# Kernel optimization log

Hardware: AMD Instinct MI355X
Metric: run time of the kernel (lower is better)

## Reference

```python
import jax, jax.numpy as jnp
import numpy as np

B, NSTEP, NSAMPLE = 16, 32, 10
EMBED, STATE, VOCAB, TOTAL = 128, 512, 32000, 8192
STD_SCALE = 0.113
EPS = 1e-5


def setup_inputs() -> dict:
    key = jax.random.key(0)
    ks = jax.random.split(key, 9)
    g = lambda k, shape: jax.random.normal(k, shape, jnp.float32) * 0.05
    return {
        "zi": jax.random.randint(ks[0], (B,), 0, TOTAL),
        "y": jax.random.randint(ks[1], (B, NSTEP), 0, VOCAB),
        "rd": jax.random.uniform(ks[2], (NSTEP, B, NSAMPLE), jnp.float32),
        "latent": g(ks[3], (TOTAL, EMBED)),
        "state_pref_W": g(ks[4], (STATE, 2 * EMBED)),
        "state_pref_b": g(ks[5], (STATE,)),
        "state_move": g(ks[6], (STATE, EMBED)),
        "vocab_W": g(ks[7], (VOCAB, EMBED)),
        "vocab_b": g(ks[8], (VOCAB,)),
    }


def reference(zi, y, rd, latent, state_pref_W, state_pref_b, state_move, vocab_W, vocab_b):
    # z: [B, NSAMPLE, D] -- latent row per batch element, repeated over samples
    z0 = jnp.repeat(latent[zi][:, None, :], NSAMPLE, axis=1)

    def step(carry, rd_t):
        z, zold, lp = carry
        # per-step normalization (torch std is unbiased, ddof=1)
        z = z / (EPS + jnp.std(z, axis=-1, ddof=1, keepdims=True)) * STD_SCALE
        pref = jnp.concatenate([zold, z], axis=-1) @ state_pref_W.T + state_pref_b  # [B,S,STATE]
        xp = jax.nn.softmax(pref, axis=-1)
        xpc = jnp.cumsum(xp, axis=-1)
        # first index where rd < cumulative prob (argmax of bool = first True)
        which = jnp.argmax(rd_t[:, :, None] < xpc, axis=-1)  # [B,S]
        xps = jnp.take_along_axis(xp, which[:, :, None], axis=-1)[..., 0]
        lp = lp + jnp.log(xps)
        mvs = state_move[which]  # [B,S,D]
        return (z + mvs, z, mvs), mvs

    init = (z0, jnp.zeros_like(z0), jnp.zeros((B, NSAMPLE), jnp.float32))
    # note: carry slot 2 of init is lp=0; fix tuple to match step outputs
    init = (z0, jnp.zeros_like(z0), jnp.zeros((B, NSAMPLE), jnp.float32))

    def step_fixed(carry, rd_t):
        z, zold, lp = carry
        z = z / (EPS + jnp.std(z, axis=-1, ddof=1, keepdims=True)) * STD_SCALE
        pref = jnp.concatenate([zold, z], axis=-1) @ state_pref_W.T + state_pref_b
        xp = jax.nn.softmax(pref, axis=-1)
        xpc = jnp.cumsum(xp, axis=-1)
        which = jnp.argmax(rd_t[:, :, None] < xpc, axis=-1)
        xps = jnp.take_along_axis(xp, which[:, :, None], axis=-1)[..., 0]
        lp = lp + jnp.log(xps)
        mvs = state_move[which]
        return (z + mvs, z, lp), mvs

    (_, _, lp), emits = jax.lax.scan(step_fixed, init, rd)  # emits: [T,B,S,D]
    emits = jnp.transpose(emits, (1, 0, 2, 3))  # [B,T,S,D]
    ys = jax.nn.log_softmax(emits @ vocab_W.T + vocab_b, axis=-1)  # [B,T,S,V]
    idx = jnp.broadcast_to(y[:, :, None, None], (B, NSTEP, NSAMPLE, 1))
    yp = jnp.take_along_axis(ys, idx, axis=-1)[..., 0]  # [B,T,S]
    return yp.mean(axis=2)  # [B,T]
```

## Files before the change

### kernel.cpp

```cpp
#include <hip/hip_runtime.h>
#include <hip/hip_bf16.h>

#define B_ 16
#define T_ 32
#define NS_ 10
#define D_ 128
#define ST_ 512
#define V_ 32000
#define NCHAIN 160

using short8  = __attribute__((ext_vector_type(8))) short;
using f32x4   = __attribute__((ext_vector_type(4))) float;
using half8   = __attribute__((ext_vector_type(8))) _Float16;
using half2v  = __attribute__((ext_vector_type(2))) _Float16;

__device__ __forceinline__ unsigned short f2bf(float f){
  unsigned u = __float_as_uint(f);
  u += 0x7FFFu + ((u >> 16) & 1u);
  return (unsigned short)(u >> 16);
}
__device__ __forceinline__ unsigned packbf(float a, float b){
  return ((unsigned)f2bf(b) << 16) | (unsigned)f2bf(a);
}
__device__ __forceinline__ unsigned short f2h(float f){
  return __builtin_bit_cast(unsigned short, (_Float16)f);
}
__device__ __forceinline__ float h2f(unsigned u, int hi){
  half2v h = __builtin_bit_cast(half2v, u);
  return (float)h[hi];
}
__device__ __forceinline__ float readlane_f(float v, int lane){
  return __int_as_float(__builtin_amdgcn_readlane(__float_as_int(v), lane));
}

#define DPPADD(x, ctrl, rm) { \
  int _t = __builtin_amdgcn_update_dpp(0, __float_as_int(x), ctrl, rm, 0xf, true); \
  x += __int_as_float(_t); }

__global__ __launch_bounds__(256) void prep_kernel(
    const int* __restrict__ zi, const float* __restrict__ latent,
    const float* __restrict__ prefW, const float* __restrict__ move,
    unsigned short* __restrict__ Hh, unsigned short* __restrict__ Lh,
    unsigned short* __restrict__ Gh,
    float* __restrict__ HU0, float* __restrict__ LU0, float* __restrict__ D0,
    float2* __restrict__ S0, float2* __restrict__ SM,
    unsigned* __restrict__ mbf, float* __restrict__ partial)
{
  if (blockIdx.x < 48){
    const int sg = blockIdx.x / 6, vc = blockIdx.x % 6;
    const int wv = threadIdx.x >> 6, lane = threadIdx.x & 63;
    const int c16 = lane & 15, q = lane >> 4;

    half8 afr[4][4];
    #pragma unroll
    for (int rt = 0; rt < 4; ++rt){
      const float* mp = move + (sg*64 + rt*16 + c16)*D_ + q*8;
      #pragma unroll
      for (int kk = 0; kk < 4; ++kk){
        float4 f0 = *(const float4*)(mp + kk*32);
        float4 f1 = *(const float4*)(mp + kk*32 + 4);
        half8 a;
        a[0]=(_Float16)f0.x; a[1]=(_Float16)f0.y; a[2]=(_Float16)f0.z; a[3]=(_Float16)f0.w;
        a[4]=(_Float16)f1.x; a[5]=(_Float16)f1.y; a[6]=(_Float16)f1.z; a[7]=(_Float16)f1.w;
        afr[rt][kk] = a;
      }
    }
    for (int it = 0; it < 4; ++it){
      const int ct = vc*256 + it*64 + wv*16 + c16;
      const float* bp; unsigned short* base; int ccol;
      if (ct < 512)      { bp = prefW + ct*256 + 128; base = Hh; ccol = ct; }
      else if (ct < 1024){ bp = prefW + (ct-512)*256; base = Lh; ccol = ct-512; }
      else               { bp = move + (ct-1024)*128; base = Gh; ccol = ct-1024; }
      half8 bfr[4];
      #pragma unroll
      for (int kk = 0; kk < 4; ++kk){
        float4 f0 = *(const float4*)(bp + q*8 + kk*32);
        float4 f1 = *(const float4*)(bp + q*8 + kk*32 + 4);
        half8 bb;
        bb[0]=(_Float16)f0.x; bb[1]=(_Float16)f0.y; bb[2]=(_Float16)f0.z; bb[3]=(_Float16)f0.w;
        bb[4]=(_Float16)f1.x; bb[5]=(_Float16)f1.y; bb[6]=(_Float16)f1.z; bb[7]=(_Float16)f1.w;
        bfr[kk] = bb;
      }
      #pragma unroll
      for (int rt = 0; rt < 4; ++rt){
        f32x4 acc = {0.f,0.f,0.f,0.f};
        #pragma unroll
        for (int kk = 0; kk < 4; ++kk)
          acc = __builtin_amdgcn_mfma_f32_16x16x32_f16(afr[rt][kk], bfr[kk], acc, 0, 0, 0);
        #pragma unroll
        for (int r = 0; r < 4; ++r){
          const int w = sg*64 + rt*16 + q*4 + r;
          base[w*ST_ + ccol] = f2h(acc[r]);
        }
      }
    }
  } else {
    const int b = blockIdx.x - 48, t = threadIdx.x;
    __shared__ float zl[128];
    if (t < 128) zl[t] = latent[zi[b]*D_ + t];
    __syncthreads();

    #pragma unroll
    for (int ii = 0; ii < 2; ++ii){
      const int sidx = t + ii*256;
      const float* wr = prefW + sidx*256;
      const float* mv = move + sidx*128;
      float hu = 0.f, lu = 0.f, d0 = 0.f;
      #pragma unroll 8
      for (int j = 0; j < 128; j += 4){
        float4 w0 = *(const float4*)(wr + j);
        float4 w1 = *(const float4*)(wr + 128 + j);
        float4 m  = *(const float4*)(mv + j);
        float4 z  = *(const float4*)(&zl[j]);
        lu += w0.x*z.x + w0.y*z.y + w0.z*z.z + w0.w*z.w;
        hu += w1.x*z.x + w1.y*z.y + w1.z*z.z + w1.w*z.w;
        d0 += m.x*z.x + m.y*z.y + m.z*z.z + m.w*z.w;
      }
      HU0[b*ST_ + sidx] = hu; LU0[b*ST_ + sidx] = lu; D0[b*ST_ + sidx] = d0;
    }
    if (t < 64){
      float a = zl[t], bb = zl[t + 64];
      float s1 = a + bb, s2 = a*a + bb*bb;
      #pragma unroll
      for (int m = 1; m < 64; m <<= 1){ s1 += __shfl_xor(s1, m, 64); s2 += __shfl_xor(s2, m, 64); }
      if (t == 0) S0[b] = make_float2(s1, s2);
    }
    {
      const int w = b*32 + (t >> 3);
      const float* mw = move + w*128 + (t & 7)*16;
      float4 m0 = *(const float4*)(mw),   m1 = *(const float4*)(mw+4);
      float4 m2 = *(const float4*)(mw+8), m3 = *(const float4*)(mw+12);
      float s1 = m0.x+m0.y+m0.z+m0.w + m1.x+m1.y+m1.z+m1.w
               + m2.x+m2.y+m2.z+m2.w + m3.x+m3.y+m3.z+m3.w;
      float s2 = m0.x*m0.x+m0.y*m0.y+m0.z*m0.z+m0.w*m0.w
               + m1.x*m1.x+m1.y*m1.y+m1.z*m1.z+m1.w*m1.w
               + m2.x*m2.x+m2.y*m2.y+m2.z*m2.z+m2.w*m2.w
               + m3.x*m3.x+m3.y*m3.y+m3.z*m3.z+m3.w*m3.w;
      #pragma unroll
      for (int m = 1; m < 8; m <<= 1){ s1 += __shfl_xor(s1, m, 64); s2 += __shfl_xor(s2, m, 64); }
      if ((t & 7) == 0) SM[w] = make_float2(s1, s2);
      unsigned* dst = mbf + w*64 + (t & 7)*8;
      dst[0] = packbf(m0.x,m0.y); dst[1] = packbf(m0.z,m0.w);
      dst[2] = packbf(m1.x,m1.y); dst[3] = packbf(m1.z,m1.w);
      dst[4] = packbf(m2.x,m2.y); dst[5] = packbf(m2.z,m2.w);
      dst[6] = packbf(m3.x,m3.y); dst[7] = packbf(m3.z,m3.w);
    }
    if (t < 32) partial[b*32 + t] = 0.f;
  }
}

__global__ __launch_bounds__(256) void work_kernel(
    const unsigned short* __restrict__ Hh, const unsigned short* __restrict__ Lh,
    const unsigned short* __restrict__ Gh, const float2* __restrict__ SM,
    const float* __restrict__ HU0, const float* __restrict__ LU0,
    const float* __restrict__ D0, const float2* __restrict__ S0,
    const float* __restrict__ prefB, const float* __restrict__ rd,
    int* __restrict__ whichOut,
    const unsigned* __restrict__ mbf, const float* __restrict__ vw,
    const float* __restrict__ vb, float* __restrict__ partial)
{
  __shared__ float les[2048];

  if (blockIdx.x < NCHAIN){
    const int t = threadIdx.x;
    if (t >= 64) return;
    const int c = blockIdx.x, b = c / NS_;
    const int l = t, t0 = l*8;

    float HU[8], LU[8], D[8], prev1[8], bias[8];
    #pragma unroll
    for (int k = 0; k < 8; k += 4){
      float4 h = *(const float4*)(HU0 + b*ST_ + t0 + k);
      float4 u = *(const float4*)(LU0 + b*ST_ + t0 + k);
      float4 d = *(const float4*)(D0  + b*ST_ + t0 + k);
      float4 bb= *(const float4*)(prefB + t0 + k);
      HU[k]=h.x; HU[k+1]=h.y; HU[k+2]=h.z; HU[k+3]=h.w;
      LU[k]=u.x; LU[k+1]=u.y; LU[k+2]=u.z; LU[k+3]=u.w;
      D[k]=d.x;  D[k+1]=d.y;  D[k+2]=d.z;  D[k+3]=d.w;
      bias[k]=bb.x; bias[k+1]=bb.y; bias[k+2]=bb.z; bias[k+3]=bb.w;
    }
    #pragma unroll
    for (int k = 0; k < 8; ++k) prev1[k] = 0.f;
    float2 s0 = S0[b];
    float S1 = s0.x, S2 = s0.y;
    float rdreg = (l < T_) ? rd[l*(B_*NS_) + c] : 0.f;

    for (int st = 0; st < T_; ++st){
      const float mean = S1 * (1.f/128.f);
      const float var  = (S2 - 128.f*mean*mean) * (1.f/127.f);
      const float sc   = 0.113f / (1e-5f + sqrtf(var));

      float cum[8]; float run = 0.f;
      #pragma unroll
      for (int k = 0; k < 8; ++k){
        float pref = fmaf(sc, HU[k], prev1[k] + bias[k]);
        run += __expf(pref);
        cum[k] = run;
      }
      float incl = run;
      DPPADD(incl, 0x111, 0xf)
      DPPADD(incl, 0x112, 0xf)
      DPPADD(incl, 0x114, 0xf)
      DPPADD(incl, 0x118, 0xf)
      DPPADD(incl, 0x142, 0xa)
      DPPADD(incl, 0x143, 0xc)
      const float total  = readlane_f(incl, 63);
      const float target = readlane_f(rdreg, st) * total;

      const bool cond = target < incl;
      const unsigned long long bal = __ballot(cond);
      const float excl = incl - run;
      int kw = 7; float dcand = D[7];
      #pragma unroll
      for (int k = 6; k >= 0; --k){
        bool ck = target < excl + cum[k];
        kw = ck ? k : kw;
        dcand = ck ? D[k] : dcand;
      }
      int which; float dW;
      if (bal){
        const int wlane = __ffsll(bal) - 1;
        which = __builtin_amdgcn_readlane(t0 + kw, wlane);
        dW    = readlane_f(dcand, wlane);
      } else {
        which = 0;
        dW    = readlane_f(D[0], 0);
      }
      if (l == 0) whichOut[c*T_ + st] = which;

      const int rb = which*ST_ + t0;
      const uint4 hq = *(const uint4*)(Hh + rb);
      const uint4 lq = *(const uint4*)(Lh + rb);
      const uint4 gq = *(const uint4*)(Gh + rb);
      const float2 sm = SM[which];
      const unsigned ha[4] = {hq.x, hq.y, hq.z, hq.w};
      const unsigned la[4] = {lq.x, lq.y, lq.z, lq.w};
      const unsigned ga[4] = {gq.x, gq.y, gq.z, gq.w};
      #pragma unroll
      for (int k = 0; k < 8; ++k){
        const float Hk = h2f(ha[k>>1], k&1);
        const float Lk = h2f(la[k>>1], k&1);
        const float Gk = h2f(ga[k>>1], k&1);
        const float p1 = sc * LU[k];
        HU[k] = fmaf(sc, HU[k], Hk);
        LU[k] = p1 + Lk;
        D[k]  = fmaf(sc, D[k], Gk);
        prev1[k] = p1;
      }
      S1 = fmaf(sc, S1, sm.x);
      S2 = fmaf(sc*sc, S2, fmaf(2.f*sc, dW, sm.y));
    }
  } else {
    const int t = threadIdx.x, lane = t & 63, wv = t >> 6;
    const int lblk = blockIdx.x - NCHAIN;

    const int vbase = lblk*128 + wv*32;
    short8 afr[2][4];
    float vbr[2][4];
    #pragma unroll
    for (int vt = 0; vt < 2; ++vt){
      const int vr = vbase + vt*16 + (lane & 15);
      const float* wp = vw + vr*D_ + (lane >> 4)*8;
      #pragma unroll
      for (int kk = 0; kk < 4; ++kk){
        float4 f0 = *(const float4*)(wp + kk*32);
        float4 f1 = *(const float4*)(wp + kk*32 + 4);
        short8 a;
        a[0]=(short)f2bf(f0.x); a[1]=(short)f2bf(f0.y);
        a[2]=(short)f2bf(f0.z); a[3]=(short)f2bf(f0.w);
        a[4]=(short)f2bf(f1.x); a[5]=(short)f2bf(f1.y);
        a[6]=(short)f2bf(f1.z); a[7]=(short)f2bf(f1.w);
        afr[vt][kk] = a;
      }
      #pragma unroll
      for (int r = 0; r < 4; ++r)
        vbr[vt][r] = vb[vbase + vt*16 + (lane >> 4)*4 + r];
    }

    const char* mb = (const char*)mbf;
    float esl[32];
    #pragma unroll
    for (int s = 0; s < 32; ++s) esl[s] = 0.f;

    #pragma unroll 4
    for (int s = 0; s < 32; ++s){
      short8 bfr[4];
      #pragma unroll
      for (int kk = 0; kk < 4; ++kk){
        const int row = s*16 + (lane & 15);
        bfr[kk] = *(const short8*)(mb + row*256 + (lane >> 4)*16 + kk*64);
      }
      #pragma unroll
      for (int vt = 0; vt < 2; ++vt){
        f32x4 acc = {0.f,0.f,0.f,0.f};
        #pragma unroll
        for (int kk = 0; kk < 4; ++kk)
          acc = __builtin_amdgcn_mfma_f32_16x16x32_bf16(afr[vt][kk], bfr[kk], acc, 0, 0, 0);
        #pragma unroll
        for (int r = 0; r < 4; ++r)
          esl[s] += __expf(acc[r] + vbr[vt][r]);
      }
    }
    #pragma unroll
    for (int s = 0; s < 32; ++s){
      esl[s] += __shfl_xor(esl[s], 16, 64);
      esl[s] += __shfl_xor(esl[s], 32, 64);
    }
    if (lane < 16){
      #pragma unroll
      for (int s = 0; s < 32; ++s) les[wv*512 + s*16 + lane] = esl[s];
    }
    __syncthreads();
    #pragma unroll
    for (int i = 0; i < 2; ++i){
      const int st = t + i*256;
      atomicAdd(&partial[st], les[st] + les[512+st] + les[1024+st] + les[1536+st]);
    }
  }
}

__global__ __launch_bounds__(256) void dots_kernel(
    const int* __restrict__ whichIn, const int* __restrict__ y,
    const float* __restrict__ move, const float* __restrict__ vw,
    const float* __restrict__ vb, const float* __restrict__ partial,
    float* __restrict__ out)
{
  const int p = blockIdx.x*4 + (threadIdx.x >> 6);
  const int lane = threadIdx.x & 63;
  const int b = p >> 5, st = p & 31;

  int w10 = 0; float ls = 0.f;
  if (lane < NS_){
    w10 = whichIn[(b*NS_ + lane)*T_ + st];
    ls  = __logf(partial[w10]);
  }
  #pragma unroll
  for (int m = 1; m < 16; m <<= 1) ls += __shfl_xor(ls, m, 64);

  float mv0 = 0.f, mv1 = 0.f;
  #pragma unroll
  for (int s = 0; s < NS_; ++s){
    const int ws = __builtin_amdgcn_readlane(w10, s);
    mv0 += move[ws*D_ + lane];
    mv1 += move[ws*D_ + 64 + lane];
  }
  const int yr = y[b*T_ + st];
  float pacc = mv0*vw[yr*D_ + lane] + mv1*vw[yr*D_ + 64 + lane];
  #pragma unroll
  for (int m = 1; m < 64; m <<= 1) pacc += __shfl_xor(pacc, m, 64);
  if (lane == 0) out[b*T_ + st] = (pacc - ls) * (1.f/NS_) + vb[yr];
}

extern "C" void kernel_launch(void* const* d_in, const int* in_sizes, int n_in,
                              void* d_out, int out_size, void* d_ws, size_t ws_size,
                              hipStream_t stream)
{
  const int*   zi     = (const int*)d_in[0];
  const int*   y      = (const int*)d_in[1];
  const float* rd     = (const float*)d_in[2];
  const float* latent = (const float*)d_in[3];
  const float* prefW  = (const float*)d_in[4];
  const float* prefB  = (const float*)d_in[5];
  const float* move   = (const float*)d_in[6];
  const float* vw     = (const float*)d_in[7];
  const float* vb     = (const float*)d_in[8];
  float* out = (float*)d_out;

  char* ws = (char*)d_ws;
  unsigned short* Hh = (unsigned short*)(ws);
  unsigned short* Lh = (unsigned short*)(ws + 524288);
  unsigned short* Gh = (unsigned short*)(ws + 1048576);
  float2* SM    = (float2*)(ws + 1572864);
  float*  HU0   = (float*)(ws + 1576960);
  float*  LU0   = (float*)(ws + 1609728);
  float*  D0    = (float*)(ws + 1642496);
  float2* S0    = (float2*)(ws + 1675264);
  float*  partial = (float*)(ws + 1675392);
  int*    which = (int*)(ws + 1677440);
  unsigned* mbf = (unsigned*)(ws + 1697920);

  hipLaunchKernelGGL(prep_kernel, dim3(64), dim3(256), 0, stream,
                     zi, latent, prefW, move, Hh, Lh, Gh,
                     HU0, LU0, D0, S0, SM, mbf, partial);
  hipLaunchKernelGGL(work_kernel, dim3(NCHAIN + 250), dim3(256), 0, stream,
                     Hh, Lh, Gh, SM, HU0, LU0, D0, S0, prefB, rd, which,
                     mbf, vw, vb, partial);
  hipLaunchKernelGGL(dots_kernel, dim3(128), dim3(256), 0, stream,
                     which, y, move, vw, vb, partial, out);
}
```

Baseline: 65.13 us.

## Fuse prep, work and dots kernels into one cooperative kernel with grid syncs

Merges the three launches into one cooperative kernel of 256 blocks, with grid-wide syncs between the prep, chain/logsumexp and output phases. If the cooperative launch fails it falls back to three launches of the same kernel. The prep matmul is spread over 192 blocks instead of 48, and the vocab logsumexp work is looped over 96 blocks instead of 250. This is meant to remove launch gaps, at the cost of grid-sync overhead and fewer blocks for the vocab phase, which now runs concurrently with the serial chains.

```diff
diff --git a/kernel.cpp b/kernel.cpp
--- a/kernel.cpp
+++ b/kernel.cpp
@@ -1,5 +1,8 @@
 #include <hip/hip_runtime.h>
 #include <hip/hip_bf16.h>
+#include <hip/hip_cooperative_groups.h>
+
+namespace cg = cooperative_groups;
 
 #define B_ 16
 #define T_ 32
@@ -8,6 +11,7 @@
 #define ST_ 512
 #define V_ 32000
 #define NCHAIN 160
+#define NBLK 256
 
 using short8  = __attribute__((ext_vector_type(8))) short;
 using f32x4   = __attribute__((ext_vector_type(4))) float;
@@ -37,36 +41,42 @@
   int _t = __builtin_amdgcn_update_dpp(0, __float_as_int(x), ctrl, rm, 0xf, true); \
   x += __int_as_float(_t); }
 
-__global__ __launch_bounds__(256) void prep_kernel(
-    const int* __restrict__ zi, const float* __restrict__ latent,
-    const float* __restrict__ prefW, const float* __restrict__ move,
+__global__ __launch_bounds__(256) void fused_kernel(
+    const int* __restrict__ zi, const int* __restrict__ y,
+    const float* __restrict__ rd, const float* __restrict__ latent,
+    const float* __restrict__ prefW, const float* __restrict__ prefB,
+    const float* __restrict__ move, const float* __restrict__ vw,
+    const float* __restrict__ vb,
     unsigned short* __restrict__ Hh, unsigned short* __restrict__ Lh,
-    unsigned short* __restrict__ Gh,
+    unsigned short* __restrict__ Gh, float2* __restrict__ SM,
     float* __restrict__ HU0, float* __restrict__ LU0, float* __restrict__ D0,
-    float2* __restrict__ S0, float2* __restrict__ SM,
-    unsigned* __restrict__ mbf, float* __restrict__ partial)
+    float2* __restrict__ S0, float* __restrict__ partial,
+    int* __restrict__ whichOut, unsigned* __restrict__ mbf,
+    float* __restrict__ out, int coop, int phase)
 {
-  if (blockIdx.x < 48){
-    const int sg = blockIdx.x / 6, vc = blockIdx.x % 6;
-    const int wv = threadIdx.x >> 6, lane = threadIdx.x & 63;
-    const int c16 = lane & 15, q = lane >> 4;
-
-    half8 afr[4][4];
-    #pragma unroll
-    for (int rt = 0; rt < 4; ++rt){
-      const float* mp = move + (sg*64 + rt*16 + c16)*D_ + q*8;
-      #pragma unroll
-      for (int kk = 0; kk < 4; ++kk){
-        float4 f0 = *(const float4*)(mp + kk*32);
-        float4 f1 = *(const float4*)(mp + kk*32 + 4);
-        half8 a;
-        a[0]=(_Float16)f0.x; a[1]=(_Float16)f0.y; a[2]=(_Float16)f0.z; a[3]=(_Float16)f0.w;
-        a[4]=(_Float16)f1.x; a[5]=(_Float16)f1.y; a[6]=(_Float16)f1.z; a[7]=(_Float16)f1.w;
-        afr[rt][kk] = a;
-      }
-    }
-    for (int it = 0; it < 4; ++it){
-      const int ct = vc*256 + it*64 + wv*16 + c16;
+  __shared__ float les[2048];
+  const int bid = blockIdx.x, t = threadIdx.x;
+  const int lane = t & 63, wv = t >> 6;
+  const int c16 = lane & 15, q = lane >> 4;
+
+  if (phase & 1){
+    if (bid < 192){
+      const int sg = bid / 24, tile = bid % 24;
+      half8 afr[4][4];
+      #pragma unroll
+      for (int rt = 0; rt < 4; ++rt){
+        const float* mp = move + (sg*64 + rt*16 + c16)*D_ + q*8;
+        #pragma unroll
+        for (int kk = 0; kk < 4; ++kk){
+          float4 f0 = *(const float4*)(mp + kk*32);
+          float4 f1 = *(const float4*)(mp + kk*32 + 4);
+          half8 a;
+          a[0]=(_Float16)f0.x; a[1]=(_Float16)f0.y; a[2]=(_Float16)f0.z; a[3]=(_Float16)f0.w;
+          a[4]=(_Float16)f1.x; a[5]=(_Float16)f1.y; a[6]=(_Float16)f1.z; a[7]=(_Float16)f1.w;
+          afr[rt][kk] = a;
+        }
+      }
+      const int ct = tile*64 + wv*16 + c16;
       const float* bp; unsigned short* base; int ccol;
       if (ct < 512)      { bp = prefW + ct*256 + 128; base = Hh; ccol = ct; }
       else if (ct < 1024){ bp = prefW + (ct-512)*256; base = Lh; ccol = ct-512; }
@@ -93,262 +103,251 @@
           base[w*ST_ + ccol] = f2h(acc[r]);
         }
       }
-    }
-  } else {
-    const int b = blockIdx.x - 48, t = threadIdx.x;
-    __shared__ float zl[128];
-    if (t < 128) zl[t] = latent[zi[b]*D_ + t];
-    __syncthreads();
-
-    #pragma unroll
-    for (int ii = 0; ii < 2; ++ii){
-      const int sidx = t + ii*256;
-      const float* wr = prefW + sidx*256;
-      const float* mv = move + sidx*128;
-      float hu = 0.f, lu = 0.f, d0 = 0.f;
-      #pragma unroll 8
-      for (int j = 0; j < 128; j += 4){
-        float4 w0 = *(const float4*)(wr + j);
-        float4 w1 = *(const float4*)(wr + 128 + j);
-        float4 m  = *(const float4*)(mv + j);
-        float4 z  = *(const float4*)(&zl[j]);
-        lu += w0.x*z.x + w0.y*z.y + w0.z*z.z + w0.w*z.w;
-        hu += w1.x*z.x + w1.y*z.y + w1.z*z.z + w1.w*z.w;
-        d0 += m.x*z.x + m.y*z.y + m.z*z.z + m.w*z.w;
-      }
-      HU0[b*ST_ + sidx] = hu; LU0[b*ST_ + sidx] = lu; D0[b*ST_ + sidx] = d0;
-    }
-    if (t < 64){
-      float a = zl[t], bb = zl[t + 64];
-      float s1 = a + bb, s2 = a*a + bb*bb;
-      #pragma unroll
-      for (int m = 1; m < 64; m <<= 1){ s1 += __shfl_xor(s1, m, 64); s2 += __shfl_xor(s2, m, 64); }
-      if (t == 0) S0[b] = make_float2(s1, s2);
-    }
-    {
-      const int w = b*32 + (t >> 3);
-      const float* mw = move + w*128 + (t & 7)*16;
-      float4 m0 = *(const float4*)(mw),   m1 = *(const float4*)(mw+4);
-      float4 m2 = *(const float4*)(mw+8), m3 = *(const float4*)(mw+12);
-      float s1 = m0.x+m0.y+m0.z+m0.w + m1.x+m1.y+m1.z+m1.w
-               + m2.x+m2.y+m2.z+m2.w + m3.x+m3.y+m3.z+m3.w;
-      float s2 = m0.x*m0.x+m0.y*m0.y+m0.z*m0.z+m0.w*m0.w
-               + m1.x*m1.x+m1.y*m1.y+m1.z*m1.z+m1.w*m1.w
-               + m2.x*m2.x+m2.y*m2.y+m2.z*m2.z+m2.w*m2.w
-               + m3.x*m3.x+m3.y*m3.y+m3.z*m3.z+m3.w*m3.w;
-      #pragma unroll
-      for (int m = 1; m < 8; m <<= 1){ s1 += __shfl_xor(s1, m, 64); s2 += __shfl_xor(s2, m, 64); }
-      if ((t & 7) == 0) SM[w] = make_float2(s1, s2);
-      unsigned* dst = mbf + w*64 + (t & 7)*8;
-      dst[0] = packbf(m0.x,m0.y); dst[1] = packbf(m0.z,m0.w);
-      dst[2] = packbf(m1.x,m1.y); dst[3] = packbf(m1.z,m1.w);
-      dst[4] = packbf(m2.x,m2.y); dst[5] = packbf(m2.z,m2.w);
-      dst[6] = packbf(m3.x,m3.y); dst[7] = packbf(m3.z,m3.w);
-    }
-    if (t < 32) partial[b*32 + t] = 0.f;
-  }
-}
-
-__global__ __launch_bounds__(256) void work_kernel(
-    const unsigned short* __restrict__ Hh, const unsigned short* __restrict__ Lh,
-    const unsigned short* __restrict__ Gh, const float2* __restrict__ SM,
-    const float* __restrict__ HU0, const float* __restrict__ LU0,
-    const float* __restrict__ D0, const float2* __restrict__ S0,
-    const float* __restrict__ prefB, const float* __restrict__ rd,
-    int* __restrict__ whichOut,
-    const unsigned* __restrict__ mbf, const float* __restrict__ vw,
-    const float* __restrict__ vb, float* __restrict__ partial)
-{
-  __shared__ float les[2048];
-
-  if (blockIdx.x < NCHAIN){
-    const int t = threadIdx.x;
-    if (t >= 64) return;
-    const int c = blockIdx.x, b = c / NS_;
-    const int l = t, t0 = l*8;
-
-    float HU[8], LU[8], D[8], prev1[8], bias[8];
-    #pragma unroll
-    for (int k = 0; k < 8; k += 4){
-      float4 h = *(const float4*)(HU0 + b*ST_ + t0 + k);
-      float4 u = *(const float4*)(LU0 + b*ST_ + t0 + k);
-      float4 d = *(const float4*)(D0  + b*ST_ + t0 + k);
-      float4 bb= *(const float4*)(prefB + t0 + k);
-      HU[k]=h.x; HU[k+1]=h.y; HU[k+2]=h.z; HU[k+3]=h.w;
-      LU[k]=u.x; LU[k+1]=u.y; LU[k+2]=u.z; LU[k+3]=u.w;
-      D[k]=d.x;  D[k+1]=d.y;  D[k+2]=d.z;  D[k+3]=d.w;
-      bias[k]=bb.x; bias[k+1]=bb.y; bias[k+2]=bb.z; bias[k+3]=bb.w;
-    }
-    #pragma unroll
-    for (int k = 0; k < 8; ++k) prev1[k] = 0.f;
-    float2 s0 = S0[b];
-    float S1 = s0.x, S2 = s0.y;
-    float rdreg = (l < T_) ? rd[l*(B_*NS_) + c] : 0.f;
-
-    for (int st = 0; st < T_; ++st){
-      const float mean = S1 * (1.f/128.f);
-      const float var  = (S2 - 128.f*mean*mean) * (1.f/127.f);
-      const float sc   = 0.113f / (1e-5f + sqrtf(var));
-
-      float cum[8]; float run = 0.f;
-      #pragma unroll
-      for (int k = 0; k < 8; ++k){
-        float pref = fmaf(sc, HU[k], prev1[k] + bias[k]);
-        run += __expf(pref);
-        cum[k] = run;
-      }
-      float incl = run;
-      DPPADD(incl, 0x111, 0xf)
-      DPPADD(incl, 0x112, 0xf)
-      DPPADD(incl, 0x114, 0xf)
-      DPPADD(incl, 0x118, 0xf)
-      DPPADD(incl, 0x142, 0xa)
-      DPPADD(incl, 0x143, 0xc)
-      const float total  = readlane_f(incl, 63);
-      const float target = readlane_f(rdreg, st) * total;
-
-      const bool cond = target < incl;
-      const unsigned long long bal = __ballot(cond);
-      const float excl = incl - run;
-      int kw = 7; float dcand = D[7];
-      #pragma unroll
-      for (int k = 6; k >= 0; --k){
-        bool ck = target < excl + cum[k];
-        kw = ck ? k : kw;
-        dcand = ck ? D[k] : dcand;
-      }
-      int which; float dW;
-      if (bal){
-        const int wlane = __ffsll(bal) - 1;
-        which = __builtin_amdgcn_readlane(t0 + kw, wlane);
-        dW    = readlane_f(dcand, wlane);
-      } else {
-        which = 0;
-        dW    = readlane_f(D[0], 0);
-      }
-      if (l == 0) whichOut[c*T_ + st] = which;
-
-      const int rb = which*ST_ + t0;
-      const uint4 hq = *(const uint4*)(Hh + rb);
-      const uint4 lq = *(const uint4*)(Lh + rb);
-      const uint4 gq = *(const uint4*)(Gh + rb);
-      const float2 sm = SM[which];
-      const unsigned ha[4] = {hq.x, hq.y, hq.z, hq.w};
-      const unsigned la[4] = {lq.x, lq.y, lq.z, lq.w};
-      const unsigned ga[4] = {gq.x, gq.y, gq.z, gq.w};
-      #pragma unroll
-      for (int k = 0; k < 8; ++k){
-        const float Hk = h2f(ha[k>>1], k&1);
-        const float Lk = h2f(la[k>>1], k&1);
-        const float Gk = h2f(ga[k>>1], k&1);
-        const float p1 = sc * LU[k];
-        HU[k] = fmaf(sc, HU[k], Hk);
-        LU[k] = p1 + Lk;
-        D[k]  = fmaf(sc, D[k], Gk);
-        prev1[k] = p1;
-      }
-      S1 = fmaf(sc, S1, sm.x);
-      S2 = fmaf(sc*sc, S2, fmaf(2.f*sc, dW, sm.y));
-    }
-  } else {
-    const int t = threadIdx.x, lane = t & 63, wv = t >> 6;
-    const int lblk = blockIdx.x - NCHAIN;
-
-    const int vbase = lblk*128 + wv*32;
-    short8 afr[2][4];
-    float vbr[2][4];
-    #pragma unroll
-    for (int vt = 0; vt < 2; ++vt){
-      const int vr = vbase + vt*16 + (lane & 15);
-      const float* wp = vw + vr*D_ + (lane >> 4)*8;
-      #pragma unroll
-      for (int kk = 0; kk < 4; ++kk){
-        float4 f0 = *(const float4*)(wp + kk*32);
-        float4 f1 = *(const float4*)(wp + kk*32 + 4);
-        short8 a;
-        a[0]=(short)f2bf(f0.x); a[1]=(short)f2bf(f0.y);
-        a[2]=(short)f2bf(f0.z); a[3]=(short)f2bf(f0.w);
-        a[4]=(short)f2bf(f1.x); a[5]=(short)f2bf(f1.y);
-        a[6]=(short)f2bf(f1.z); a[7]=(short)f2bf(f1.w);
-        afr[vt][kk] = a;
-      }
-      #pragma unroll
-      for (int r = 0; r < 4; ++r)
-        vbr[vt][r] = vb[vbase + vt*16 + (lane >> 4)*4 + r];
-    }
-
-    const char* mb = (const char*)mbf;
-    float esl[32];
-    #pragma unroll
-    for (int s = 0; s < 32; ++s) esl[s] = 0.f;
-
-    #pragma unroll 4
-    for (int s = 0; s < 32; ++s){
-      short8 bfr[4];
-      #pragma unroll
-      for (int kk = 0; kk < 4; ++kk){
-        const int row = s*16 + (lane & 15);
-        bfr[kk] = *(const short8*)(mb + row*256 + (lane >> 4)*16 + kk*64);
-      }
-      #pragma unroll
-      for (int vt = 0; vt < 2; ++vt){
-        f32x4 acc = {0.f,0.f,0.f,0.f};
-        #pragma unroll
-        for (int kk = 0; kk < 4; ++kk)
-          acc = __builtin_amdgcn_mfma_f32_16x16x32_bf16(afr[vt][kk], bfr[kk], acc, 0, 0, 0);
-        #pragma unroll
-        for (int r = 0; r < 4; ++r)
-          esl[s] += __expf(acc[r] + vbr[vt][r]);
-      }
-    }
-    #pragma unroll
-    for (int s = 0; s < 32; ++s){
-      esl[s] += __shfl_xor(esl[s], 16, 64);
-      esl[s] += __shfl_xor(esl[s], 32, 64);
-    }
-    if (lane < 16){
-      #pragma unroll
-      for (int s = 0; s < 32; ++s) les[wv*512 + s*16 + lane] = esl[s];
-    }
-    __syncthreads();
-    #pragma unroll
-    for (int i = 0; i < 2; ++i){
-      const int st = t + i*256;
-      atomicAdd(&partial[st], les[st] + les[512+st] + les[1024+st] + les[1536+st]);
+    } else if (bid < 208){
+      const int b = bid - 192;
+      float* zl = les;
+      if (t < 128) zl[t] = latent[zi[b]*D_ + t];
+      __syncthreads();
+
+      #pragma unroll
+      for (int ii = 0; ii < 2; ++ii){
+        const int sidx = t + ii*256;
+        const float* wr = prefW + sidx*256;
+        const float* mv = move + sidx*128;
+        float hu = 0.f, lu = 0.f, d0 = 0.f;
+        #pragma unroll 8
+        for (int j = 0; j < 128; j += 4){
+          float4 w0 = *(const float4*)(wr + j);
+          float4 w1 = *(const float4*)(wr + 128 + j);
+          float4 m  = *(const float4*)(mv + j);
+          float4 z  = *(const float4*)(&zl[j]);
+          lu += w0.x*z.x + w0.y*z.y + w0.z*z.z + w0.w*z.w;
+          hu += w1.x*z.x + w1.y*z.y + w1.z*z.z + w1.w*z.w;
+          d0 += m.x*z.x + m.y*z.y + m.z*z.z + m.w*z.w;
+        }
+        HU0[b*ST_ + sidx] = hu; LU0[b*ST_ + sidx] = lu; D0[b*ST_ + sidx] = d0;
+      }
+      if (t < 64){
+        float a = zl[t], bb = zl[t + 64];
+        float s1 = a + bb, s2 = a*a + bb*bb;
+        #pragma unroll
+        for (int m = 1; m < 64; m <<= 1){ s1 += __shfl_xor(s1, m, 64); s2 += __shfl_xor(s2, m, 64); }
+        if (t == 0) S0[b] = make_float2(s1, s2);
+      }
+      {
+        const int w = b*32 + (t >> 3);
+        const float* mw = move + w*128 + (t & 7)*16;
+        float4 m0 = *(const float4*)(mw),   m1 = *(const float4*)(mw+4);
+        float4 m2 = *(const float4*)(mw+8), m3 = *(const float4*)(mw+12);
+        float s1 = m0.x+m0.y+m0.z+m0.w + m1.x+m1.y+m1.z+m1.w
+                 + m2.x+m2.y+m2.z+m2.w + m3.x+m3.y+m3.z+m3.w;
+        float s2 = m0.x*m0.x+m0.y*m0.y+m0.z*m0.z+m0.w*m0.w
+                 + m1.x*m1.x+m1.y*m1.y+m1.z*m1.z+m1.w*m1.w
+                 + m2.x*m2.x+m2.y*m2.y+m2.z*m2.z+m2.w*m2.w
+                 + m3.x*m3.x+m3.y*m3.y+m3.z*m3.z+m3.w*m3.w;
+        #pragma unroll
+        for (int m = 1; m < 8; m <<= 1){ s1 += __shfl_xor(s1, m, 64); s2 += __shfl_xor(s2, m, 64); }
+        if ((t & 7) == 0) SM[w] = make_float2(s1, s2);
+        unsigned* dst = mbf + w*64 + (t & 7)*8;
+        dst[0] = packbf(m0.x,m0.y); dst[1] = packbf(m0.z,m0.w);
+        dst[2] = packbf(m1.x,m1.y); dst[3] = packbf(m1.z,m1.w);
+        dst[4] = packbf(m2.x,m2.y); dst[5] = packbf(m2.z,m2.w);
+        dst[6] = packbf(m3.x,m3.y); dst[7] = packbf(m3.z,m3.w);
+      }
+      if (t < 32) partial[b*32 + t] = 0.f;
     }
   }
-}
-
-__global__ __launch_bounds__(256) void dots_kernel(
-    const int* __restrict__ whichIn, const int* __restrict__ y,
-    const float* __restrict__ move, const float* __restrict__ vw,
-    const float* __restrict__ vb, const float* __restrict__ partial,
-    float* __restrict__ out)
-{
-  const int p = blockIdx.x*4 + (threadIdx.x >> 6);
-  const int lane = threadIdx.x & 63;
-  const int b = p >> 5, st = p & 31;
-
-  int w10 = 0; float ls = 0.f;
-  if (lane < NS_){
-    w10 = whichIn[(b*NS_ + lane)*T_ + st];
-    ls  = __logf(partial[w10]);
+
+  if (coop){ __threadfence(); cg::this_grid().sync(); }
+
+  if (phase & 2){
+    if (bid < NCHAIN){
+      if (t < 64){
+        const int c = bid, b = c / NS_;
+        const int l = t, t0 = l*8;
+
+        float HU[8], LU[8], D[8], prev1[8], bias[8];
+        #pragma unroll
+        for (int k = 0; k < 8; k += 4){
+          float4 h = *(const float4*)(HU0 + b*ST_ + t0 + k);
+          float4 u = *(const float4*)(LU0 + b*ST_ + t0 + k);
+          float4 d = *(const float4*)(D0  + b*ST_ + t0 + k);
+          float4 bb= *(const float4*)(prefB + t0 + k);
+          HU[k]=h.x; HU[k+1]=h.y; HU[k+2]=h.z; HU[k+3]=h.w;
+          LU[k]=u.x; LU[k+1]=u.y; LU[k+2]=u.z; LU[k+3]=u.w;
+          D[k]=d.x;  D[k+1]=d.y;  D[k+2]=d.z;  D[k+3]=d.w;
+          bias[k]=bb.x; bias[k+1]=bb.y; bias[k+2]=bb.z; bias[k+3]=bb.w;
+        }
+        #pragma unroll
+        for (int k = 0; k < 8; ++k) prev1[k] = 0.f;
+        float2 s0 = S0[b];
+        float S1 = s0.x, S2 = s0.y;
+        float rdreg = (l < T_) ? rd[l*(B_*NS_) + c] : 0.f;
+
+        for (int st = 0; st < T_; ++st){
+          const float mean = S1 * (1.f/128.f);
+          const float var  = (S2 - 128.f*mean*mean) * (1.f/127.f);
+          const float sc   = 0.113f / (1e-5f + sqrtf(var));
+
+          float cum[8]; float run = 0.f;
+          #pragma unroll
+          for (int k = 0; k < 8; ++k){
+            float pref = fmaf(sc, HU[k], prev1[k] + bias[k]);
+            run += __expf(pref);
+            cum[k] = run;
+          }
+          float incl = run;
+          DPPADD(incl, 0x111, 0xf)
+          DPPADD(incl, 0x112, 0xf)
+          DPPADD(incl, 0x114, 0xf)
+          DPPADD(incl, 0x118, 0xf)
+          DPPADD(incl, 0x142, 0xa)
+          DPPADD(incl, 0x143, 0xc)
+          const float total  = readlane_f(incl, 63);
+          const float target = readlane_f(rdreg, st) * total;
+
+          const bool cond = target < incl;
+          const unsigned long long bal = __ballot(cond);
+          const float excl = incl - run;
+          int kw = 7; float dcand = D[7];
+          #pragma unroll
+          for (int k = 6; k >= 0; --k){
+            bool ck = target < excl + cum[k];
+            kw = ck ? k : kw;
+            dcand = ck ? D[k] : dcand;
+          }
+          int which; float dW;
+          if (bal){
+            const int wlane = __ffsll(bal) - 1;
+            which = __builtin_amdgcn_readlane(t0 + kw, wlane);
+            dW    = readlane_f(dcand, wlane);
+          } else {
+            which = 0;
+            dW    = readlane_f(D[0], 0);
+          }
+          if (l == 0) whichOut[c*T_ + st] = which;
+
+          const int rb = which*ST_ + t0;
+          const uint4 hq = *(const uint4*)(Hh + rb);
+          const uint4 lq = *(const uint4*)(Lh + rb);
+          const uint4 gq = *(const uint4*)(Gh + rb);
+          const float2 sm = SM[which];
+          const unsigned ha[4] = {hq.x, hq.y, hq.z, hq.w};
+          const unsigned la[4] = {lq.x, lq.y, lq.z, lq.w};
+          const unsigned ga[4] = {gq.x, gq.y, gq.z, gq.w};
+          #pragma unroll
+          for (int k = 0; k < 8; ++k){
+            const float Hk = h2f(ha[k>>1], k&1);
+            const float Lk = h2f(la[k>>1], k&1);
+            const float Gk = h2f(ga[k>>1], k&1);
+            const float p1 = sc * LU[k];
+            HU[k] = fmaf(sc, HU[k], Hk);
+            LU[k] = p1 + Lk;
+            D[k]  = fmaf(sc, D[k], Gk);
+            prev1[k] = p1;
+          }
+          S1 = fmaf(sc, S1, sm.x);
+          S2 = fmaf(sc*sc, S2, fmaf(2.f*sc, dW, sm.y));
+        }
+      }
+    } else {
+      const char* mb = (const char*)mbf;
+      for (int u = bid - NCHAIN; u < 250; u += NBLK - NCHAIN){
+        const int vbase = u*128 + wv*32;
+        short8 afr[2][4];
+        float vbr[2][4];
+        #pragma unroll
+        for (int vt = 0; vt < 2; ++vt){
+          const int vr = vbase + vt*16 + c16;
+          const float* wp = vw + vr*D_ + q*8;
+          #pragma unroll
+          for (int kk = 0; kk < 4; ++kk){
+            float4 f0 = *(const float4*)(wp + kk*32);
+            float4 f1 = *(const float4*)(wp + kk*32 + 4);
+            short8 a;
+            a[0]=(short)f2bf(f0.x); a[1]=(short)f2bf(f0.y);
+            a[2]=(short)f2bf(f0.z); a[3]=(short)f2bf(f0.w);
+            a[4]=(short)f2bf(f1.x); a[5]=(short)f2bf(f1.y);
+            a[6]=(short)f2bf(f1.z); a[7]=(short)f2bf(f1.w);
+            afr[vt][kk] = a;
+          }
+          #pragma unroll
+          for (int r = 0; r < 4; ++r)
+            vbr[vt][r] = vb[vbase + vt*16 + q*4 + r];
+        }
+
+        float esl[32];
+        #pragma unroll
+        for (int s = 0; s < 32; ++s) esl[s] = 0.f;
+
+        #pragma unroll
+        for (int s = 0; s < 32; ++s){
+          short8 bfr[4];
+          #pragma unroll
+          for (int kk = 0; kk < 4; ++kk){
+            const int row = s*16 + c16;
+            bfr[kk] = *(const short8*)(mb + row*256 + q*16 + kk*64);
+          }
+          #pragma unroll
+          for (int vt = 0; vt < 2; ++vt){
+            f32x4 acc = {0.f,0.f,0.f,0.f};
+            #pragma unroll
+            for (int kk = 0; kk < 4; ++kk)
+              acc = __builtin_amdgcn_mfma_f32_16x16x32_bf16(afr[vt][kk], bfr[kk], acc, 0, 0, 0);
+            #pragma unroll
+            for (int r = 0; r < 4; ++r)
+              esl[s] += __expf(acc[r] + vbr[vt][r]);
+          }
+        }
+        #pragma unroll
+        for (int s = 0; s < 32; ++s){
+          esl[s] += __shfl_xor(esl[s], 16, 64);
+          esl[s] += __shfl_xor(esl[s], 32, 64);
+        }
+        if (lane < 16){
+          #pragma unroll
+          for (int s = 0; s < 32; ++s) les[wv*512 + s*16 + lane] = esl[s];
+        }
+        __syncthreads();
+        #pragma unroll
+        for (int i = 0; i < 2; ++i){
+          const int st = t + i*256;
+          atomicAdd(&partial[st], les[st] + les[512+st] + les[1024+st] + les[1536+st]);
+        }
+        __syncthreads();
+      }
+    }
   }
-  #pragma unroll
-  for (int m = 1; m < 16; m <<= 1) ls += __shfl_xor(ls, m, 64);
-
-  float mv0 = 0.f, mv1 = 0.f;
-  #pragma unroll
-  for (int s = 0; s < NS_; ++s){
-    const int ws = __builtin_amdgcn_readlane(w10, s);
-    mv0 += move[ws*D_ + lane];
-    mv1 += move[ws*D_ + 64 + lane];
+
+  if (coop){ __threadfence(); cg::this_grid().sync(); }
+
+  if (phase & 4){
+    if (bid < 128){
+      const int p = bid*4 + wv;
+      const int b = p >> 5, st = p & 31;
+
+      int w10 = 0; float ls = 0.f;
+      if (lane < NS_){
+        w10 = whichOut[(b*NS_ + lane)*T_ + st];
+        ls  = __logf(partial[w10]);
+      }
+      #pragma unroll
+      for (int m = 1; m < 16; m <<= 1) ls += __shfl_xor(ls, m, 64);
+
+      float mv0 = 0.f, mv1 = 0.f;
+      #pragma unroll
+      for (int s = 0; s < NS_; ++s){
+        const int ws = __builtin_amdgcn_readlane(w10, s);
+        mv0 += move[ws*D_ + lane];
+        mv1 += move[ws*D_ + 64 + lane];
+      }
+      const int yr = y[b*T_ + st];
+      float pacc = mv0*vw[yr*D_ + lane] + mv1*vw[yr*D_ + 64 + lane];
+      #pragma unroll
+      for (int m = 1; m < 64; m <<= 1) pacc += __shfl_xor(pacc, m, 64);
+      if (lane == 0) out[b*T_ + st] = (pacc - ls) * (1.f/NS_) + vb[yr];
+    }
   }
-  const int yr = y[b*T_ + st];
-  float pacc = mv0*vw[yr*D_ + lane] + mv1*vw[yr*D_ + 64 + lane];
-  #pragma unroll
-  for (int m = 1; m < 64; m <<= 1) pacc += __shfl_xor(pacc, m, 64);
-  if (lane == 0) out[b*T_ + st] = (pacc - ls) * (1.f/NS_) + vb[yr];
 }
 
 extern "C" void kernel_launch(void* const* d_in, const int* in_sizes, int n_in,
@@ -379,12 +378,30 @@
   int*    which = (int*)(ws + 1677440);
   unsigned* mbf = (unsigned*)(ws + 1697920);
 
-  hipLaunchKernelGGL(prep_kernel, dim3(64), dim3(256), 0, stream,
-                     zi, latent, prefW, move, Hh, Lh, Gh,
-                     HU0, LU0, D0, S0, SM, mbf, partial);
-  hipLaunchKernelGGL(work_kernel, dim3(NCHAIN + 250), dim3(256), 0, stream,
-                     Hh, Lh, Gh, SM, HU0, LU0, D0, S0, prefB, rd, which,
-                     mbf, vw, vb, partial);
-  hipLaunchKernelGGL(dots_kernel, dim3(128), dim3(256), 0, stream,
-                     which, y, move, vw, vb, partial, out);
-}
+  int coop1 = 1, phase7 = 7;
+  void* args[] = {
+    (void*)&zi, (void*)&y, (void*)&rd, (void*)&latent, (void*)&prefW,
+    (void*)&prefB, (void*)&move, (void*)&vw, (void*)&vb,
+    (void*)&Hh, (void*)&Lh, (void*)&Gh, (void*)&SM,
+    (void*)&HU0, (void*)&LU0, (void*)&D0, (void*)&S0,
+    (void*)&partial, (void*)&which, (void*)&mbf, (void*)&out,
+    (void*)&coop1, (void*)&phase7
+  };
+  hipError_t e = hipLaunchCooperativeKernel((const void*)fused_kernel,
+                                            dim3(NBLK), dim3(256), args, 0, stream);
+  if (e != hipSuccess){
+    (void)hipGetLastError();
+    hipLaunchKernelGGL(fused_kernel, dim3(NBLK), dim3(256), 0, stream,
+                       zi, y, rd, latent, prefW, prefB, move, vw, vb,
+                       Hh, Lh, Gh, SM, HU0, LU0, D0, S0, partial, which, mbf,
+                       out, 0, 1);
+    hipLaunchKernelGGL(fused_kernel, dim3(NBLK), dim3(256), 0, stream,
+                       zi, y, rd, latent, prefW, prefB, move, vw, vb,
+                       Hh, Lh, Gh, SM, HU0, LU0, D0, S0, partial, which, mbf,
+                       out, 0, 2);
+    hipLaunchKernelGGL(fused_kernel, dim3(NBLK), dim3(256), 0, stream,
+                       zi, y, rd, latent, prefW, prefB, move, vw, vb,
+                       Hh, Lh, Gh, SM, HU0, LU0, D0, S0, partial, which, mbf,
+                       out, 0, 4);
+  }
+}
```

Result: slower. 219.2 us (+236.5%).
